# Optimization experiments

Measured on AMD Instinct MI355X. Metric: run time of the kernel, lower is better.

The kernel has to match this reference:

```python
import jax, jax.numpy as jnp
import numpy as np

PATCH = 24  # self.current_patch
STRIDE = PATCH // 2


def _conv(x, w, b):
    # NCHW conv, SAME padding, stride 1 (= Conv2d(k=3, padding=1))
    y = jax.lax.conv_general_dilated(x, w, (1, 1), 'SAME',
                                     dimension_numbers=('NCHW', 'OIHW', 'NCHW'))
    return y + b[None, :, None, None]


def setup_inputs() -> dict:
    key = jax.random.key(0)
    ks = jax.random.split(key, 9)
    b, c, h, w = 2, 64, 192, 192
    s = 0.05  # keep sigmoid/tanh unsaturated
    return {
        'source': jax.random.normal(ks[0], (b, c, h, w), jnp.float32),
        'target': jax.random.normal(ks[1], (b, c, h, w), jnp.float32),
        # deform_net params (128->512->256->1)
        'W1': jax.random.normal(ks[2], (512, 128, 3, 3), jnp.float32) * s,
        'b1': jnp.zeros((512,), jnp.float32),
        'W2': jax.random.normal(ks[3], (256, 512, 3, 3), jnp.float32) * s,
        'b2': jnp.zeros((256,), jnp.float32),
        'W3': jax.random.normal(ks[4], (1, 256, 3, 3), jnp.float32) * s,
        'b3': jnp.zeros((1,), jnp.float32),
        # reg_net params (128->512->64->1); original declared 256 in-ch (bug), fixed to 128
        'Wr1': jax.random.normal(ks[5], (512, 128, 3, 3), jnp.float32) * s,
        'br1': jnp.zeros((512,), jnp.float32),
        'Wr2': jax.random.normal(ks[6], (64, 512, 3, 3), jnp.float32) * s,
        'br2': jnp.zeros((64,), jnp.float32),
        'Wr3': jax.random.normal(ks[7], (1, 64, 3, 3), jnp.float32) * s,
        'br3': jnp.zeros((1,), jnp.float32),
    }


def _attention(src, tgt, W1, b1, W2, b2, W3, b3):
    b, c, h, w = src.shape
    p, st = PATCH, STRIDE
    nH = (h - p) // st + 1
    nW = (w - p) // st + 1
    # patch gather indices
    r_idx = jnp.arange(nH)[:, None] * st + jnp.arange(p)[None, :]  # [nH, p]
    c_idx = jnp.arange(nW)[:, None] * st + jnp.arange(p)[None, :]  # [nW, p]
    # [b, c, nH, nW, p, p]
    def gather(x):
        return x[:, :, r_idx[:, None, :, None], c_idx[None, :, None, :]]
    ps = gather(src)
    pt = gather(tgt)
    # -> [b*nH*nW, 2c, p, p]  (one big batched conv replaces the python loop)
    pair = jnp.concatenate([ps, pt], axis=1)            # [b, 2c, nH, nW, p, p]
    pair = pair.transpose(0, 2, 3, 1, 4, 5).reshape(b * nH * nW, 2 * c, p, p)
    x = jax.nn.relu(_conv(pair, W1, b1))
    x = jax.nn.relu(_conv(x, W2, b2))
    score = jax.nn.sigmoid(_conv(x, W3, b3))            # [b*nH*nW, 1, p, p]
    score = score.reshape(b, nH, nW, 1, p, p).transpose(0, 3, 1, 2, 4, 5)  # [b,1,nH,nW,p,p]
    # overlap-add scatter (duplicate indices accumulate)
    R = jnp.broadcast_to(r_idx[:, None, :, None], (nH, nW, p, p))
    C = jnp.broadcast_to(c_idx[None, :, None, :], (nH, nW, p, p))
    att = jnp.zeros((b, 1, h, w), src.dtype).at[:, :, R, C].add(score)
    cnt = jnp.zeros((b, 1, h, w), src.dtype).at[:, :, R, C].add(1.0)
    return att / jnp.maximum(cnt, 1.0)


def reference(source, target, W1, b1, W2, b2, W3, b3, Wr1, br1, Wr2, br2, Wr3, br3):
    attention_map = _attention(source, target, W1, b1, W2, b2, W3, b3)
    x = jnp.concatenate([source, target], axis=1)       # [b, 128, h, w]
    x = jax.nn.relu(_conv(x, Wr1, br1))
    x = jax.nn.relu(_conv(x, Wr2, br2))
    registered = jnp.tanh(_conv(x, Wr3, br3))           # [b, 1, h, w]
    return registered, attention_map
```

## Files before the change

kernel.cpp:

```cpp
#include <hip/hip_runtime.h>
#include <cmath>

typedef _Float16 half8  __attribute__((ext_vector_type(8)));
typedef _Float16 half4v __attribute__((ext_vector_type(4)));
typedef float    float4v __attribute__((ext_vector_type(4)));

template<int MT, int NT>
__global__ __launch_bounds__(256, 2)
void mfma_conv(const _Float16* __restrict__ in, const _Float16* __restrict__ Wg,
               const float* __restrict__ bias, _Float16* __restrict__ out,
               int CI, int CO, int RSin, int RSout, int IMG, int NB, int NC)
{
    __shared__ __align__(16) _Float16 sW[9 * MT * 64 * 8];

    const int tid  = threadIdx.x;
    const int wave = tid >> 6;
    const int lane = tid & 63;
    const int ll   = lane & 15;
    const int quad = lane >> 4;

    const int NSUB = NC * (9 / NT);
    const int id   = blockIdx.x;
    const int xcd  = id & 7;
    const int slot = id >> 3;
    const int unit = (slot / NSUB) * 8 + xcd;
    const int rem  = slot % NSUB;
    const int pxb  = rem / NC;
    const int co_t = rem % NC;
    if (unit >= NB) return;
    const int co0 = co_t * (MT * 16);
    const int pbase = pxb * (NT * 64) + wave * (NT * 16);

    size_t in_base, out_base;
    int TY = 0, TX = 0;
    if (IMG) {
        int tile = unit & 63, b = unit >> 6;
        TY = (tile >> 3) * 24; TX = (tile & 7) * 24;
        in_base  = (size_t)b * RSin * RSin * CI;
        out_base = (size_t)b * RSout * RSout * CO;
    } else {
        in_base  = (size_t)unit * 676 * CI;
        out_base = (size_t)unit * 676 * CO;
    }

    int b_off[NT];
    #pragma unroll
    for (int nt = 0; nt < NT; ++nt) {
        int p = pbase + nt * 16 + ll;
        b_off[nt] = ((TY + p / 24) * RSin + (TX + p % 24)) * CI;
    }
    int tapoff[9];
    #pragma unroll
    for (int dy = 0; dy < 3; ++dy)
        #pragma unroll
        for (int dx = 0; dx < 3; ++dx)
            tapoff[dy * 3 + dx] = (dy * RSin + dx) * CI;

    float4v acc[MT][NT];
    #pragma unroll
    for (int mt = 0; mt < MT; ++mt)
        #pragma unroll
        for (int nt = 0; nt < NT; ++nt)
            acc[mt][nt] = (float4v){0.f, 0.f, 0.f, 0.f};

    for (int ci0 = 0; ci0 < CI; ci0 += 32) {
        __syncthreads();
        for (int c = tid; c < 9 * MT * 64; c += 256) {
            int lane_s = c & 63;
            int mtt = c >> 6;
            int mt = mtt % MT, t = mtt / MT;
            *(uint4*)&sW[(size_t)c * 8] =
                *(const uint4*)&Wg[((size_t)(co0 + mt * 16 + (lane_s & 15)) * 9 + t) * CI
                                   + ci0 + (lane_s >> 4) * 8];
        }
        __syncthreads();

        const _Float16* inp = in + in_base + ci0 + quad * 8;
        #pragma unroll
        for (int t = 0; t < 9; ++t) {
            half8 a[MT];
            #pragma unroll
            for (int mt = 0; mt < MT; ++mt)
                a[mt] = *(const half8*)&sW[((t * MT + mt) * 64 + lane) * 8];
            const int toff = tapoff[t];
            #pragma unroll
            for (int nt = 0; nt < NT; ++nt) {
                half8 b = *(const half8*)(inp + b_off[nt] + toff);
                #pragma unroll
                for (int mt = 0; mt < MT; ++mt)
                    acc[mt][nt] = __builtin_amdgcn_mfma_f32_16x16x32_f16(
                        a[mt], b, acc[mt][nt], 0, 0, 0);
            }
        }
    }

    #pragma unroll
    for (int mt = 0; mt < MT; ++mt) {
        float4v bs = *(const float4v*)&bias[co0 + mt * 16 + quad * 4];
        #pragma unroll
        for (int nt = 0; nt < NT; ++nt) {
            int p = pbase + nt * 16 + ll;
            size_t ooff = out_base
                + (size_t)((TY + p / 24 + 1) * RSout + (TX + p % 24) + 1) * CO
                + co0 + mt * 16 + quad * 4;
            float4v v = acc[mt][nt];
            half4v h;
            h.x = (_Float16)fmaxf(v.x + bs.x, 0.f);
            h.y = (_Float16)fmaxf(v.y + bs.y, 0.f);
            h.z = (_Float16)fmaxf(v.z + bs.z, 0.f);
            h.w = (_Float16)fmaxf(v.w + bs.w, 0.f);
            *(half4v*)(out + ooff) = h;
        }
    }
}

static inline int swiz_grid(int NB, int NC, int PXB) {
    return ((NB + 7) & ~7) * NC * PXB;
}

template<int MODE, int ACT>
__global__ __launch_bounds__(256, 2)
void mfma_score(const _Float16* __restrict__ in, const _Float16* __restrict__ W16,
                const float* __restrict__ bias, float* __restrict__ outp,
                int CI, int RSI, int NB)
{
    __shared__ __align__(16) _Float16 sW[9 * 16 * 32];

    const int tid  = threadIdx.x;
    const int wave = tid >> 6;
    const int lane = tid & 63;
    const int ll   = lane & 15;
    const int quad = lane >> 4;

    const int blk = blockIdx.x;
    if (blk >= NB) return;

    size_t in_base;
    int ty = 0, tx = 0, bb = 0;
    if (MODE == 2) {
        bb = blk >> 6; int tile = blk & 63; ty = tile >> 3; tx = tile & 7;
        in_base = (size_t)bb * RSI * RSI * CI;
    } else {
        in_base = (size_t)blk * 676 * CI;
    }

    int b_off[9];
    #pragma unroll
    for (int nt = 0; nt < 9; ++nt) {
        int p = wave * 144 + nt * 16 + ll;
        int py = p / 24, px = p % 24;
        b_off[nt] = (MODE == 2) ? ((ty * 24 + py) * RSI + (tx * 24 + px)) * CI
                                : (py * RSI + px) * CI;
    }

    float4v acc[9];
    #pragma unroll
    for (int nt = 0; nt < 9; ++nt) acc[nt] = (float4v){0.f, 0.f, 0.f, 0.f};

    for (int ci0 = 0; ci0 < CI; ci0 += 32) {
        __syncthreads();
        for (int c = tid; c < 9 * 16 * 4; c += 256) {
            int q = c & 3, tco = c >> 2;
            int t = tco >> 4, co = tco & 15;
            *(uint4*)&sW[tco * 32 + q * 8] =
                *(const uint4*)&W16[((size_t)co * 9 + t) * CI + ci0 + q * 8];
        }
        __syncthreads();

        const _Float16* inp = in + in_base + ci0 + quad * 8;
        for (int dy = 0; dy < 3; ++dy)
            for (int dx = 0; dx < 3; ++dx) {
                const int t = dy * 3 + dx;
                const int toff = (dy * RSI + dx) * CI;
                half8 a = *(const half8*)&sW[(t * 16 + ll) * 32 + quad * 8];
                #pragma unroll
                for (int nt = 0; nt < 9; ++nt) {
                    half8 b = *(const half8*)(inp + b_off[nt] + toff);
                    acc[nt] = __builtin_amdgcn_mfma_f32_16x16x32_f16(a, b, acc[nt], 0, 0, 0);
                }
            }
    }

    if (quad == 0) {
        float bv = bias[0];
        #pragma unroll
        for (int nt = 0; nt < 9; ++nt) {
            int p = wave * 144 + nt * 16 + ll;
            float v = acc[nt].x + bv;
            if (ACT == 1) {
                outp[(size_t)blk * 576 + p] = 1.f / (1.f + expf(-v));
            } else {
                int y = ty * 24 + p / 24, x = tx * 24 + p % 24;
                outp[(size_t)bb * 36864 + y * 192 + x] = tanhf(v);
            }
        }
    }
}

__global__ __launch_bounds__(256)
void build_x16i(const float* __restrict__ src, const float* __restrict__ tgt,
                _Float16* __restrict__ X)
{
    int idx = blockIdx.x * 256 + threadIdx.x;
    int q = idx & 15, pid = idx >> 4;
    if (pid >= 2 * 36864) return;
    int b = pid / 36864, r = pid % 36864;
    int y = r / 192, x = r % 192;
    half8 h;
    #pragma unroll
    for (int j = 0; j < 8; ++j) {
        int ch = q * 8 + j;
        const float* im = (ch < 64) ? src : tgt;
        h[j] = (_Float16)im[(size_t)(b * 64 + (ch & 63)) * 36864 + r];
    }
    *(half8*)&X[(((size_t)b * 194 + y + 1) * 194 + (x + 1)) * 128 + q * 8] = h;
}

__global__ __launch_bounds__(256)
void cvt_w(const float* __restrict__ src, _Float16* __restrict__ dst, int CO, int CI)
{
    int idx = blockIdx.x * 256 + threadIdx.x;
    if (idx >= CO * 9 * CI) return;
    int ci = idx % CI, t = (idx / CI) % 9, co = idx / (9 * CI);
    dst[idx] = (_Float16)src[((size_t)co * CI + ci) * 9 + t];
}

__global__ __launch_bounds__(256)
void cvt_pad16(const float* __restrict__ src, _Float16* __restrict__ dst, int CI)
{
    int idx = blockIdx.x * 256 + threadIdx.x;
    if (idx >= 16 * 9 * CI) return;
    int ci = idx % CI, t = (idx / CI) % 9, co = idx / (9 * CI);
    dst[idx] = (co == 0) ? (_Float16)src[(size_t)ci * 9 + t] : (_Float16)0.0f;
}

__global__ __launch_bounds__(256)
void g_patch(const _Float16* __restrict__ X, _Float16* __restrict__ P1, int p0, int nP)
{
    int idx = blockIdx.x * 256 + threadIdx.x;
    if (idx >= nP * 676 * 16) return;
    int q = idx & 15, t2 = idx >> 4;
    int r676 = t2 % 676, pl = t2 / 676;
    int pr = r676 / 26, pc = r676 % 26;
    int P = p0 + pl;
    int b = P / 225, rem = P % 225, pi = rem / 15, pj = rem % 15;
    uint4 v = {0u, 0u, 0u, 0u};
    if (pr >= 1 && pr <= 24 && pc >= 1 && pc <= 24)
        v = *(const uint4*)&X[(((size_t)b * 194 + pi * 12 + pr) * 194 + (pj * 12 + pc)) * 128 + q * 8];
    *(uint4*)&P1[((size_t)pl * 676 + r676) * 128 + q * 8] = v;
}

__global__ __launch_bounds__(256)
void ring_zero(_Float16* __restrict__ buf, int npatch, int RS, int CI)
{
    int c8 = CI >> 3;
    int RC = 2 * RS + 2 * (RS - 2);
    int idx = blockIdx.x * 256 + threadIdx.x;
    if (idx >= npatch * RC * c8) return;
    int q = idx % c8, rp = (idx / c8) % RC, pl = idx / (c8 * RC);
    int r, c;
    if (rp < RS)            { r = 0;      c = rp; }
    else if (rp < 2 * RS)   { r = RS - 1; c = rp - RS; }
    else {
        int s = rp - 2 * RS, half = RS - 2;
        if (s < half) { r = s + 1;        c = 0; }
        else          { r = s - half + 1; c = RS - 1; }
    }
    uint4 z = {0u, 0u, 0u, 0u};
    *(uint4*)&buf[((size_t)pl * RS * RS + r * RS + c) * CI + q * 8] = z;
}

__global__ __launch_bounds__(256)
void att_finalize(const float* __restrict__ score, float* __restrict__ out)
{
    int idx = blockIdx.x * 256 + threadIdx.x;
    if (idx >= 2 * 36864) return;
    int b = idx / 36864, r = idx % 36864;
    int y = r / 192, x = r % 192;
    int i_lo = (y >= 24) ? (y - 12) / 12 : 0;
    int i_hi = min(14, y / 12);
    int j_lo = (x >= 24) ? (x - 12) / 12 : 0;
    int j_hi = min(14, x / 12);
    float s = 0.f; int cnt = 0;
    for (int i = i_lo; i <= i_hi; ++i)
        for (int j = j_lo; j <= j_hi; ++j) {
            s += score[(((size_t)b * 15 + i) * 15 + j) * 576 + (y - 12 * i) * 24 + (x - 12 * j)];
            ++cnt;
        }
    out[idx] = s / (float)cnt;
}

extern "C" void kernel_launch(void* const* d_in, const int* in_sizes, int n_in,
                              void* d_out, int out_size, void* d_ws, size_t ws_size,
                              hipStream_t stream)
{
    const float* src = (const float*)d_in[0];
    const float* tgt = (const float*)d_in[1];
    const float* W1  = (const float*)d_in[2];  const float* b1  = (const float*)d_in[3];
    const float* W2  = (const float*)d_in[4];  const float* b2  = (const float*)d_in[5];
    const float* W3  = (const float*)d_in[6];  const float* b3  = (const float*)d_in[7];
    const float* Wr1 = (const float*)d_in[8];  const float* br1 = (const float*)d_in[9];
    const float* Wr2 = (const float*)d_in[10]; const float* br2 = (const float*)d_in[11];
    const float* Wr3 = (const float*)d_in[12]; const float* br3 = (const float*)d_in[13];
    float* out = (float*)d_out;

    _Float16* ws = (_Float16*)d_ws;
    size_t o = 0;
    _Float16* X16i = ws + o; o += (size_t)2 * 194 * 194 * 128;
    _Float16* W1h  = ws + o; o += (size_t)512 * 9 * 128;
    _Float16* W2h  = ws + o; o += (size_t)256 * 9 * 512;
    _Float16* Wr1h = ws + o; o += (size_t)512 * 9 * 128;
    _Float16* Wr2h = ws + o; o += (size_t)64 * 9 * 512;
    _Float16* W3p  = ws + o; o += (size_t)16 * 9 * 256;
    _Float16* Wr3p = ws + o; o += (size_t)16 * 9 * 64;
    float*    score = (float*)(ws + o); o += 2 * 259200;
    const size_t fixed_h = o;

    const size_t per_patch_h = (size_t)676 * (128 + 512 + 256);
    const size_t regA_h = (size_t)2 * 194 * 194 * 512;
    const size_t regB_h = (size_t)2 * 194 * 194 * 64;
    size_t h_avail = ws_size / 2;
    int P = 50;
    {
        size_t n450 = 450 * per_patch_h; if (n450 < regA_h + regB_h) n450 = regA_h + regB_h;
        size_t n150 = 150 * per_patch_h; if (n150 < regA_h + regB_h) n150 = regA_h + regB_h;
        if (h_avail >= fixed_h + n450)      P = 450;
        else if (h_avail >= fixed_h + n150) P = 150;
    }
    const int nchunks = 450 / P;

    _Float16* P1 = ws + fixed_h;
    _Float16* D1 = P1 + (size_t)P * 676 * 128;
    _Float16* D2 = D1 + (size_t)P * 676 * 512;

    ring_zero<<<(2 * 772 * 16 + 255) / 256, 256, 0, stream>>>(X16i, 2, 194, 128);
    build_x16i<<<4608, 256, 0, stream>>>(src, tgt, X16i);
    cvt_w<<<2304, 256, 0, stream>>>(W1,  W1h,  512, 128);
    cvt_w<<<4608, 256, 0, stream>>>(W2,  W2h,  256, 512);
    cvt_w<<<2304, 256, 0, stream>>>(Wr1, Wr1h, 512, 128);
    cvt_w<<<1152, 256, 0, stream>>>(Wr2, Wr2h, 64,  512);
    cvt_pad16<<<(16 * 9 * 256 + 255) / 256, 256, 0, stream>>>(W3,  W3p,  256);
    cvt_pad16<<<(16 * 9 * 64  + 255) / 256, 256, 0, stream>>>(Wr3, Wr3p, 64);

    ring_zero<<<(P * 100 * 64 + 255) / 256, 256, 0, stream>>>(D1, P, 26, 512);
    ring_zero<<<(P * 100 * 32 + 255) / 256, 256, 0, stream>>>(D2, P, 26, 256);
    for (int c = 0; c < nchunks; ++c) {
        int p0 = c * P;
        g_patch<<<(P * 676 * 16 + 255) / 256, 256, 0, stream>>>(X16i, P1, p0, P);
        mfma_conv<8, 3><<<swiz_grid(P, 4, 3), 256, 0, stream>>>(
            P1, W1h, b1, D1, 128, 512, 26, 26, 0, P, 4);
        mfma_conv<8, 3><<<swiz_grid(P, 2, 3), 256, 0, stream>>>(
            D1, W2h, b2, D2, 512, 256, 26, 26, 0, P, 2);
        mfma_score<1, 1><<<P, 256, 0, stream>>>(D2, W3p, b3, score + (size_t)p0 * 576, 256, 26, P);
    }
    att_finalize<<<288, 256, 0, stream>>>(score, out + 73728);

    if (P >= 150) {
        _Float16* A1 = ws + fixed_h;
        _Float16* A2 = A1 + regA_h;
        ring_zero<<<(2 * 772 * 64 + 255) / 256, 256, 0, stream>>>(A1, 2, 194, 512);
        ring_zero<<<(2 * 772 * 8  + 255) / 256, 256, 0, stream>>>(A2, 2, 194, 64);
        mfma_conv<4, 9><<<swiz_grid(128, 8, 1), 256, 0, stream>>>(
            X16i, Wr1h, br1, A1, 128, 512, 194, 194, 1, 128, 8);
        mfma_conv<2, 9><<<swiz_grid(128, 2, 1), 256, 0, stream>>>(
            A1, Wr2h, br2, A2, 512, 64, 194, 194, 1, 128, 2);
        mfma_score<2, 2><<<128, 256, 0, stream>>>(A2, Wr3p, br3, out, 64, 194, 128);
    } else {
        _Float16* A1 = ws + fixed_h;
        _Float16* A2 = A1 + (size_t)194 * 194 * 512;
        for (int b = 0; b < 2; ++b) {
            ring_zero<<<(772 * 64 + 255) / 256, 256, 0, stream>>>(A1, 1, 194, 512);
            ring_zero<<<(772 * 8  + 255) / 256, 256, 0, stream>>>(A2, 1, 194, 64);
            mfma_conv<4, 9><<<swiz_grid(64, 8, 1), 256, 0, stream>>>(
                X16i + (size_t)b * 194 * 194 * 128, Wr1h, br1, A1,
                128, 512, 194, 194, 1, 64, 8);
            mfma_conv<2, 9><<<swiz_grid(64, 2, 1), 256, 0, stream>>>(
                A1, Wr2h, br2, A2, 512, 64, 194, 194, 1, 64, 2);
            mfma_score<2, 2><<<64, 256, 0, stream>>>(A2, Wr3p, br3, out + (size_t)b * 36864, 64, 194, 64);
        }
    }
}
```

Baseline: 2.499 ms.

## Fuse patch gather into first conv and retile reg-net and score kernels

Removes the g_patch kernel and the P1 staging buffer: the first attention conv now reads directly from the padded full image, applying per-pixel edge masks to zero out taps that fall outside the 24x24 patch. The freed workspace lowers per-patch memory needs, which may allow larger chunk sizes. Separately, the reg-net convs switch from MT=4/NT=9 and MT=2/NT=9 tiling to MT=8/NT=3 and MT=4/NT=3, and the score kernels split each unit across three blocks for more parallelism. The tradeoff is extra masking ALU work and strided image reads in place of contiguous patch buffers.

```diff
diff --git a/kernel.cpp b/kernel.cpp
--- a/kernel.cpp
+++ b/kernel.cpp
@@ -5,11 +5,11 @@
 typedef _Float16 half4v __attribute__((ext_vector_type(4)));
 typedef float    float4v __attribute__((ext_vector_type(4)));
 
-template<int MT, int NT>
+template<int MT, int NT, int MODE>
 __global__ __launch_bounds__(256, 2)
 void mfma_conv(const _Float16* __restrict__ in, const _Float16* __restrict__ Wg,
                const float* __restrict__ bias, _Float16* __restrict__ out,
-               int CI, int CO, int RSin, int RSout, int IMG, int NB, int NC)
+               int CI, int CO, int RSin, int RSout, int NB, int NC, int p0)
 {
     __shared__ __align__(16) _Float16 sW[9 * MT * 64 * 8];
 
@@ -33,28 +33,42 @@
 
     size_t in_base, out_base;
     int TY = 0, TX = 0;
-    if (IMG) {
+    int b_off[NT], edge[NT];
+    if (MODE == 0) {
+        int pat = p0 + unit;
+        int bb = pat / 225, remp = pat % 225;
+        int pi = remp / 15, pj = remp % 15;
+        in_base  = (size_t)bb * RSin * RSin * CI;
+        out_base = (size_t)unit * 676 * CO;
+        #pragma unroll
+        for (int nt = 0; nt < NT; ++nt) {
+            int p = pbase + nt * 16 + ll;
+            int py = p / 24, px = p % 24;
+            b_off[nt] = ((pi * 12 + py) * RSin + (pj * 12 + px)) * CI;
+            edge[nt] = (py == 0 ? 1 : 0) | (py == 23 ? 2 : 0)
+                     | (px == 0 ? 4 : 0) | (px == 23 ? 8 : 0);
+        }
+    } else if (MODE == 1) {
+        in_base  = (size_t)unit * 676 * CI;
+        out_base = (size_t)unit * 676 * CO;
+        #pragma unroll
+        for (int nt = 0; nt < NT; ++nt) {
+            int p = pbase + nt * 16 + ll;
+            b_off[nt] = ((p / 24) * RSin + (p % 24)) * CI;
+            edge[nt] = 0;
+        }
+    } else {
         int tile = unit & 63, b = unit >> 6;
         TY = (tile >> 3) * 24; TX = (tile & 7) * 24;
         in_base  = (size_t)b * RSin * RSin * CI;
         out_base = (size_t)b * RSout * RSout * CO;
-    } else {
-        in_base  = (size_t)unit * 676 * CI;
-        out_base = (size_t)unit * 676 * CO;
-    }
-
-    int b_off[NT];
-    #pragma unroll
-    for (int nt = 0; nt < NT; ++nt) {
-        int p = pbase + nt * 16 + ll;
-        b_off[nt] = ((TY + p / 24) * RSin + (TX + p % 24)) * CI;
-    }
-    int tapoff[9];
-    #pragma unroll
-    for (int dy = 0; dy < 3; ++dy)
-        #pragma unroll
-        for (int dx = 0; dx < 3; ++dx)
-            tapoff[dy * 3 + dx] = (dy * RSin + dx) * CI;
+        #pragma unroll
+        for (int nt = 0; nt < NT; ++nt) {
+            int p = pbase + nt * 16 + ll;
+            b_off[nt] = ((TY + p / 24) * RSin + (TX + p % 24)) * CI;
+            edge[nt] = 0;
+        }
+    }
 
     float4v acc[MT][NT];
     #pragma unroll
@@ -77,19 +91,33 @@
 
         const _Float16* inp = in + in_base + ci0 + quad * 8;
         #pragma unroll
-        for (int t = 0; t < 9; ++t) {
-            half8 a[MT];
+        for (int dy = 0; dy < 3; ++dy) {
             #pragma unroll
-            for (int mt = 0; mt < MT; ++mt)
-                a[mt] = *(const half8*)&sW[((t * MT + mt) * 64 + lane) * 8];
-            const int toff = tapoff[t];
-            #pragma unroll
-            for (int nt = 0; nt < NT; ++nt) {
-                half8 b = *(const half8*)(inp + b_off[nt] + toff);
+            for (int dx = 0; dx < 3; ++dx) {
+                const int t = dy * 3 + dx;
+                const int toff = (dy * RSin + dx) * CI;
+                const int emask = (dy == 0 ? 1 : 0) | (dy == 2 ? 2 : 0)
+                                | (dx == 0 ? 4 : 0) | (dx == 2 ? 8 : 0);
+                half8 a[MT];
                 #pragma unroll
                 for (int mt = 0; mt < MT; ++mt)
-                    acc[mt][nt] = __builtin_amdgcn_mfma_f32_16x16x32_f16(
-                        a[mt], b, acc[mt][nt], 0, 0, 0);
+                    a[mt] = *(const half8*)&sW[((t * MT + mt) * 64 + lane) * 8];
+                #pragma unroll
+                for (int nt = 0; nt < NT; ++nt) {
+                    uint4 raw = *(const uint4*)(inp + b_off[nt] + toff);
+                    if (MODE == 0) {
+                        bool z = (edge[nt] & emask) != 0;
+                        raw.x = z ? 0u : raw.x;
+                        raw.y = z ? 0u : raw.y;
+                        raw.z = z ? 0u : raw.z;
+                        raw.w = z ? 0u : raw.w;
+                    }
+                    half8 b = *(half8*)&raw;
+                    #pragma unroll
+                    for (int mt = 0; mt < MT; ++mt)
+                        acc[mt][nt] = __builtin_amdgcn_mfma_f32_16x16x32_f16(
+                            a[mt], b, acc[mt][nt], 0, 0, 0);
+                }
             }
         }
     }
@@ -118,11 +146,11 @@
     return ((NB + 7) & ~7) * NC * PXB;
 }
 
-template<int MODE, int ACT>
+template<int MODE, int ACT, int NT>
 __global__ __launch_bounds__(256, 2)
 void mfma_score(const _Float16* __restrict__ in, const _Float16* __restrict__ W16,
                 const float* __restrict__ bias, float* __restrict__ outp,
-                int CI, int RSI, int NB)
+                int CI, int RSI, int NB, int PXB)
 {
     __shared__ __align__(16) _Float16 sW[9 * 16 * 32];
 
@@ -132,30 +160,30 @@
     const int ll   = lane & 15;
     const int quad = lane >> 4;
 
-    const int blk = blockIdx.x;
-    if (blk >= NB) return;
+    const int unit = blockIdx.x / PXB;
+    const int pxb  = blockIdx.x % PXB;
+    if (unit >= NB) return;
+    const int pbase = pxb * (NT * 64) + wave * (NT * 16);
 
     size_t in_base;
     int ty = 0, tx = 0, bb = 0;
     if (MODE == 2) {
-        bb = blk >> 6; int tile = blk & 63; ty = tile >> 3; tx = tile & 7;
+        bb = unit >> 6; int tile = unit & 63; ty = (tile >> 3) * 24; tx = (tile & 7) * 24;
         in_base = (size_t)bb * RSI * RSI * CI;
     } else {
-        in_base = (size_t)blk * 676 * CI;
-    }
-
-    int b_off[9];
-    #pragma unroll
-    for (int nt = 0; nt < 9; ++nt) {
-        int p = wave * 144 + nt * 16 + ll;
-        int py = p / 24, px = p % 24;
-        b_off[nt] = (MODE == 2) ? ((ty * 24 + py) * RSI + (tx * 24 + px)) * CI
-                                : (py * RSI + px) * CI;
-    }
-
-    float4v acc[9];
-    #pragma unroll
-    for (int nt = 0; nt < 9; ++nt) acc[nt] = (float4v){0.f, 0.f, 0.f, 0.f};
+        in_base = (size_t)unit * 676 * CI;
+    }
+
+    int b_off[NT];
+    #pragma unroll
+    for (int nt = 0; nt < NT; ++nt) {
+        int p = pbase + nt * 16 + ll;
+        b_off[nt] = ((ty + p / 24) * RSI + (tx + p % 24)) * CI;
+    }
+
+    float4v acc[NT];
+    #pragma unroll
+    for (int nt = 0; nt < NT; ++nt) acc[nt] = (float4v){0.f, 0.f, 0.f, 0.f};
 
     for (int ci0 = 0; ci0 < CI; ci0 += 32) {
         __syncthreads();
@@ -174,7 +202,7 @@
                 const int toff = (dy * RSI + dx) * CI;
                 half8 a = *(const half8*)&sW[(t * 16 + ll) * 32 + quad * 8];
                 #pragma unroll
-                for (int nt = 0; nt < 9; ++nt) {
+                for (int nt = 0; nt < NT; ++nt) {
                     half8 b = *(const half8*)(inp + b_off[nt] + toff);
                     acc[nt] = __builtin_amdgcn_mfma_f32_16x16x32_f16(a, b, acc[nt], 0, 0, 0);
                 }
@@ -184,13 +212,13 @@
     if (quad == 0) {
         float bv = bias[0];
         #pragma unroll
-        for (int nt = 0; nt < 9; ++nt) {
-            int p = wave * 144 + nt * 16 + ll;
+        for (int nt = 0; nt < NT; ++nt) {
+            int p = pbase + nt * 16 + ll;
             float v = acc[nt].x + bv;
             if (ACT == 1) {
-                outp[(size_t)blk * 576 + p] = 1.f / (1.f + expf(-v));
+                outp[(size_t)unit * 576 + p] = 1.f / (1.f + expf(-v));
             } else {
-                int y = ty * 24 + p / 24, x = tx * 24 + p % 24;
+                int y = ty + p / 24, x = tx + p % 24;
                 outp[(size_t)bb * 36864 + y * 192 + x] = tanhf(v);
             }
         }
@@ -232,22 +260,6 @@
     if (idx >= 16 * 9 * CI) return;
     int ci = idx % CI, t = (idx / CI) % 9, co = idx / (9 * CI);
     dst[idx] = (co == 0) ? (_Float16)src[(size_t)ci * 9 + t] : (_Float16)0.0f;
-}
-
-__global__ __launch_bounds__(256)
-void g_patch(const _Float16* __restrict__ X, _Float16* __restrict__ P1, int p0, int nP)
-{
-    int idx = blockIdx.x * 256 + threadIdx.x;
-    if (idx >= nP * 676 * 16) return;
-    int q = idx & 15, t2 = idx >> 4;
-    int r676 = t2 % 676, pl = t2 / 676;
-    int pr = r676 / 26, pc = r676 % 26;
-    int P = p0 + pl;
-    int b = P / 225, rem = P % 225, pi = rem / 15, pj = rem % 15;
-    uint4 v = {0u, 0u, 0u, 0u};
-    if (pr >= 1 && pr <= 24 && pc >= 1 && pc <= 24)
-        v = *(const uint4*)&X[(((size_t)b * 194 + pi * 12 + pr) * 194 + (pj * 12 + pc)) * 128 + q * 8];
-    *(uint4*)&P1[((size_t)pl * 676 + r676) * 128 + q * 8] = v;
 }
 
 __global__ __launch_bounds__(256)
@@ -316,7 +328,7 @@
     float*    score = (float*)(ws + o); o += 2 * 259200;
     const size_t fixed_h = o;
 
-    const size_t per_patch_h = (size_t)676 * (128 + 512 + 256);
+    const size_t per_patch_h = (size_t)676 * (512 + 256);
     const size_t regA_h = (size_t)2 * 194 * 194 * 512;
     const size_t regB_h = (size_t)2 * 194 * 194 * 64;
     size_t h_avail = ws_size / 2;
@@ -329,8 +341,7 @@
     }
     const int nchunks = 450 / P;
 
-    _Float16* P1 = ws + fixed_h;
-    _Float16* D1 = P1 + (size_t)P * 676 * 128;
+    _Float16* D1 = ws + fixed_h;
     _Float16* D2 = D1 + (size_t)P * 676 * 512;
 
     ring_zero<<<(2 * 772 * 16 + 255) / 256, 256, 0, stream>>>(X16i, 2, 194, 128);
@@ -346,37 +357,39 @@
     ring_zero<<<(P * 100 * 32 + 255) / 256, 256, 0, stream>>>(D2, P, 26, 256);
     for (int c = 0; c < nchunks; ++c) {
         int p0 = c * P;
-        g_patch<<<(P * 676 * 16 + 255) / 256, 256, 0, stream>>>(X16i, P1, p0, P);
-        mfma_conv<8, 3><<<swiz_grid(P, 4, 3), 256, 0, stream>>>(
-            P1, W1h, b1, D1, 128, 512, 26, 26, 0, P, 4);
-        mfma_conv<8, 3><<<swiz_grid(P, 2, 3), 256, 0, stream>>>(
-            D1, W2h, b2, D2, 512, 256, 26, 26, 0, P, 2);
-        mfma_score<1, 1><<<P, 256, 0, stream>>>(D2, W3p, b3, score + (size_t)p0 * 576, 256, 26, P);
+        mfma_conv<8, 3, 0><<<swiz_grid(P, 4, 3), 256, 0, stream>>>(
+            X16i, W1h, b1, D1, 128, 512, 194, 26, P, 4, p0);
+        mfma_conv<8, 3, 1><<<swiz_grid(P, 2, 3), 256, 0, stream>>>(
+            D1, W2h, b2, D2, 512, 256, 26, 26, P, 2, 0);
+        mfma_score<1, 1, 3><<<P * 3, 256, 0, stream>>>(
+            D2, W3p, b3, score + (size_t)p0 * 576, 256, 26, P, 3);
     }
     att_finalize<<<288, 256, 0, stream>>>(score, out + 73728);
 
-    if (P >= 150) {
+    {
         _Float16* A1 = ws + fixed_h;
-        _Float16* A2 = A1 + regA_h;
-        ring_zero<<<(2 * 772 * 64 + 255) / 256, 256, 0, stream>>>(A1, 2, 194, 512);
-        ring_zero<<<(2 * 772 * 8  + 255) / 256, 256, 0, stream>>>(A2, 2, 194, 64);
-        mfma_conv<4, 9><<<swiz_grid(128, 8, 1), 256, 0, stream>>>(
-            X16i, Wr1h, br1, A1, 128, 512, 194, 194, 1, 128, 8);
-        mfma_conv<2, 9><<<swiz_grid(128, 2, 1), 256, 0, stream>>>(
-            A1, Wr2h, br2, A2, 512, 64, 194, 194, 1, 128, 2);
-        mfma_score<2, 2><<<128, 256, 0, stream>>>(A2, Wr3p, br3, out, 64, 194, 128);
-    } else {
-        _Float16* A1 = ws + fixed_h;
-        _Float16* A2 = A1 + (size_t)194 * 194 * 512;
-        for (int b = 0; b < 2; ++b) {
-            ring_zero<<<(772 * 64 + 255) / 256, 256, 0, stream>>>(A1, 1, 194, 512);
-            ring_zero<<<(772 * 8  + 255) / 256, 256, 0, stream>>>(A2, 1, 194, 64);
-            mfma_conv<4, 9><<<swiz_grid(64, 8, 1), 256, 0, stream>>>(
-                X16i + (size_t)b * 194 * 194 * 128, Wr1h, br1, A1,
-                128, 512, 194, 194, 1, 64, 8);
-            mfma_conv<2, 9><<<swiz_grid(64, 2, 1), 256, 0, stream>>>(
-                A1, Wr2h, br2, A2, 512, 64, 194, 194, 1, 64, 2);
-            mfma_score<2, 2><<<64, 256, 0, stream>>>(A2, Wr3p, br3, out + (size_t)b * 36864, 64, 194, 64);
-        }
-    }
-}
+        _Float16* A2 = A1 + ((P >= 150) ? regA_h : (size_t)194 * 194 * 512);
+        if (P >= 150) {
+            ring_zero<<<(2 * 772 * 64 + 255) / 256, 256, 0, stream>>>(A1, 2, 194, 512);
+            ring_zero<<<(2 * 772 * 8  + 255) / 256, 256, 0, stream>>>(A2, 2, 194, 64);
+            mfma_conv<8, 3, 2><<<swiz_grid(128, 4, 3), 256, 0, stream>>>(
+                X16i, Wr1h, br1, A1, 128, 512, 194, 194, 128, 4, 0);
+            mfma_conv<4, 3, 2><<<swiz_grid(128, 1, 3), 256, 0, stream>>>(
+                A1, Wr2h, br2, A2, 512, 64, 194, 194, 128, 1, 0);
+            mfma_score<2, 2, 3><<<128 * 3, 256, 0, stream>>>(
+                A2, Wr3p, br3, out, 64, 194, 128, 3);
+        } else {
+            for (int b = 0; b < 2; ++b) {
+                ring_zero<<<(772 * 64 + 255) / 256, 256, 0, stream>>>(A1, 1, 194, 512);
+                ring_zero<<<(772 * 8  + 255) / 256, 256, 0, stream>>>(A2, 1, 194, 64);
+                mfma_conv<8, 3, 2><<<swiz_grid(64, 4, 3), 256, 0, stream>>>(
+                    X16i + (size_t)b * 194 * 194 * 128, Wr1h, br1, A1,
+                    128, 512, 194, 194, 64, 4, 0);
+                mfma_conv<4, 3, 2><<<swiz_grid(64, 1, 3), 256, 0, stream>>>(
+                    A1, Wr2h, br2, A2, 512, 64, 194, 194, 64, 1, 0);
+                mfma_score<2, 2, 3><<<64 * 3, 256, 0, stream>>>(
+                    A2, Wr3p, br3, out + (size_t)b * 36864, 64, 194, 64, 3);
+            }
+        }
+    }
+}
```

Result: faster. 2.304 ms (-7.8%).
